# Kernel optimization log

Measured on AMD Instinct MI355X. Metric: run time of the kernel, lower is better.

## Reference

```python
import jax, jax.numpy as jnp
import numpy as np

D_MODEL = 1024
NUM_HEADS = 16
D_K = D_MODEL // NUM_HEADS
THETA = 10000.0
BATCH, SEQ = 2, 2048


def _rope(xh, pos):
    # xh: (..., h, s, d_k), pos: (s,) int
    half = D_K // 2
    inv_freq = THETA ** (-jnp.arange(half, dtype=jnp.float32) * 2.0 / D_K)  # (half,)
    ang = pos.astype(jnp.float32)[:, None] * inv_freq[None, :]              # (s, half)
    cos, sin = jnp.cos(ang), jnp.sin(ang)
    x1 = xh[..., 0::2]  # (..., h, s, half)
    x2 = xh[..., 1::2]
    r1 = x1 * cos - x2 * sin
    r2 = x1 * sin + x2 * cos
    out = jnp.stack([r1, r2], axis=-1)            # (..., h, s, half, 2)
    return out.reshape(xh.shape)


def setup_inputs() -> dict:
    key = jax.random.key(0)
    k1, k2, k3 = jax.random.split(key, 3)
    scale_qkv = (6.0 / (3 * D_MODEL + D_MODEL)) ** 0.5  # xavier uniform bound
    scale_o = (6.0 / (2 * D_MODEL)) ** 0.5
    return {
        "x": jax.random.normal(k1, (BATCH, SEQ, D_MODEL), dtype=jnp.float32),
        "token_positions": jnp.arange(SEQ, dtype=jnp.int64 if jax.config.jax_enable_x64 else jnp.int32),
        "qkv_proj": jax.random.uniform(k2, (3 * D_MODEL, D_MODEL), jnp.float32, -scale_qkv, scale_qkv),
        "o_proj": jax.random.uniform(k3, (D_MODEL, D_MODEL), jnp.float32, -scale_o, scale_o),
    }


def reference(x, token_positions, qkv_proj, o_proj):
    # fused QKV projection: x @ qkv_proj^T
    qkv = jnp.einsum('bsd,ed->bse', x, qkv_proj)          # (b, s, 3*d_model)
    q, k, v = jnp.split(qkv, 3, axis=-1)

    def to_heads(t):
        b, s, _ = t.shape
        return t.reshape(b, s, NUM_HEADS, D_K).transpose(0, 2, 1, 3)  # (b, h, s, d_k)

    qh, kh, vh = to_heads(q), to_heads(k), to_heads(v)
    qh = _rope(qh, token_positions)
    kh = _rope(kh, token_positions)

    scores = jnp.einsum('bhqd,bhkd->bhqk', qh, kh) / (D_K ** 0.5)
    s = x.shape[-2]
    causal = jnp.tril(jnp.ones((s, s), dtype=bool))
    scores = jnp.where(causal, scores, -jnp.inf)
    attn = jax.nn.softmax(scores, axis=-1)
    out = jnp.einsum('bhqk,bhkd->bhqd', attn, vh)          # (b, h, s, d_k)
    out = out.transpose(0, 2, 1, 3).reshape(x.shape[0], s, D_MODEL)
    return jnp.einsum('bsd,od->bso', out, o_proj)
```

## Files before the change

kernel.cpp:

```cpp
#include <hip/hip_runtime.h>
#include <hip/hip_bf16.h>
#include <math.h>

typedef __bf16 bf16_t;
typedef __attribute__((ext_vector_type(2))) __bf16 bf16x2;
typedef __attribute__((ext_vector_type(4))) __bf16 bf16x4;
typedef __attribute__((ext_vector_type(8))) __bf16 bf16x8;
typedef __attribute__((ext_vector_type(4))) float f32x4;

#define BATCH  2
#define SEQ    2048
#define DMODEL 1024
#define NHEADS 16
#define DK     64

typedef const __attribute__((address_space(1))) void* gas_t;
typedef __attribute__((address_space(3))) void* las_t;

#define X_N (BATCH * SEQ * DMODEL)
#define W_N (3 * DMODEL * DMODEL)
#define O_N (DMODEL * DMODEL)

__global__ __launch_bounds__(256) void convert_kernel(
    const float* __restrict__ x, const float* __restrict__ w, const float* __restrict__ o,
    bf16_t* __restrict__ xb, bf16_t* __restrict__ wb, bf16_t* __restrict__ ob)
{
    const int gid = blockIdx.x * 256 + threadIdx.x;
    const float* src; bf16_t* dst; int base = gid * 8;
    if (base < X_N)                { src = x; dst = xb; }
    else if (base < X_N + W_N)     { src = w; dst = wb; base -= X_N; }
    else                           { src = o; dst = ob; base -= X_N + W_N; }
    const f32x4 lo = *(const f32x4*)(src + base);
    const f32x4 hi = *(const f32x4*)(src + base + 4);
    bf16x8 r;
    r[0] = (bf16_t)lo[0]; r[1] = (bf16_t)lo[1]; r[2] = (bf16_t)lo[2]; r[3] = (bf16_t)lo[3];
    r[4] = (bf16_t)hi[0]; r[5] = (bf16_t)hi[1]; r[6] = (bf16_t)hi[2]; r[7] = (bf16_t)hi[3];
    *(bf16x8*)(dst + base) = r;
}

__global__ __launch_bounds__(512) void qkv_gemm_kernel(
    const bf16_t* __restrict__ x, const bf16_t* __restrict__ w,
    const int* __restrict__ pos,
    bf16_t* __restrict__ qo, bf16_t* __restrict__ ko, bf16_t* __restrict__ vt)
{
    __shared__ bf16_t Abuf[2][256 * 64];
    __shared__ bf16_t Bbuf[2][192 * 64];

    const int tid  = threadIdx.x;
    const int lane = tid & 63;
    const int l15  = lane & 15, quad = lane >> 4;
    const int l7   = l15 & 7;
    const int wv   = tid >> 6;
    const int wr   = wv >> 2;
    const int wc   = wv & 3;

    const int bid = blockIdx.x;
    const int xcd = bid & 7, tt = bid >> 3;
    const int yh  = xcd >> 1, ch = xcd & 1;
    const int bx  = ch * 8 + (tt & 7);
    const int by  = yh * 4 + (tt >> 3);
    const int rowBase = by * 256;
    const int colBase = bx * 192;

    const int r0   = tid >> 3;
    const int scol = ((tid & 7) ^ (r0 & 7)) * 8;
    const bf16_t* Ax = x + (size_t)(rowBase + r0) * DMODEL + scol;
    const bf16_t* Bx = w + (size_t)(colBase + r0) * DMODEL + scol;

    f32x4 acc[8][3] = {};

#define STAGE(kt, bufi)                                                          \
    {                                                                            \
        const int k0_ = (kt) * 64;                                               \
        _Pragma("unroll")                                                        \
        for (int l = 0; l < 4; ++l)                                              \
            __builtin_amdgcn_global_load_lds(                                    \
                (gas_t)(Ax + (size_t)(l * 64) * DMODEL + k0_),                   \
                (las_t)(&Abuf[bufi][(l * 512 + tid) * 8]), 16, 0, 0);            \
        _Pragma("unroll")                                                        \
        for (int l = 0; l < 3; ++l)                                              \
            __builtin_amdgcn_global_load_lds(                                    \
                (gas_t)(Bx + (size_t)(l * 64) * DMODEL + k0_),                   \
                (las_t)(&Bbuf[bufi][(l * 512 + tid) * 8]), 16, 0, 0);            \
    }

    STAGE(0, 0)
    STAGE(1, 1)
    asm volatile("s_waitcnt vmcnt(7)" ::: "memory");
    __builtin_amdgcn_s_barrier();
    __builtin_amdgcn_sched_barrier(0);

    for (int t = 0; t < 16; ++t) {
        const int buf = t & 1;
#pragma unroll
        for (int kk = 0; kk < 2; ++kk) {
            const int sw = ((kk * 4 + quad) ^ l7) * 8;
            bf16x8 bfr[3];
#pragma unroll
            for (int j = 0; j < 3; ++j)
                bfr[j] = *(const bf16x8*)&Bbuf[buf][(wc * 48 + j * 16 + l15) * 64 + sw];
            __builtin_amdgcn_s_setprio(1);
#pragma unroll
            for (int i = 0; i < 8; ++i) {
                const bf16x8 af = *(const bf16x8*)&Abuf[buf][(wr * 128 + i * 16 + l15) * 64 + sw];
#pragma unroll
                for (int j = 0; j < 3; ++j)
                    acc[i][j] = __builtin_amdgcn_mfma_f32_16x16x32_bf16(af, bfr[j], acc[i][j], 0, 0, 0);
            }
            __builtin_amdgcn_s_setprio(0);
        }
        __builtin_amdgcn_s_barrier();
        __builtin_amdgcn_sched_barrier(0);
        if (t + 2 < 16) {
            STAGE(t + 2, buf)
            asm volatile("s_waitcnt vmcnt(7)" ::: "memory");
        } else {
            asm volatile("s_waitcnt vmcnt(0)" ::: "memory");
        }
        __builtin_amdgcn_s_barrier();
        __builtin_amdgcn_sched_barrier(0);
    }
#undef STAGE

#pragma unroll
    for (int j = 0; j < 3; ++j) {
        const int colj = colBase + wc * 48 + j * 16;
        const int part = colj >> 10;
        const int h    = (colj & 1023) >> 6;
        const int d    = (colj & 63) + l15;
        bf16_t* op = (part == 0) ? qo : (part == 1) ? ko : vt;
        if (part < 2) {
            const float invf  = exp2f(-(float)(d >> 1) * 0.4152410118609203f);
            const float psign = (d & 1) ? 1.f : -1.f;
#pragma unroll
            for (int i = 0; i < 8; ++i) {
#pragma unroll
                for (int r = 0; r < 4; ++r) {
                    const int m = rowBase + wr * 128 + i * 16 + quad * 4 + r;
                    const int b = m >> 11;
                    const int s = m & (SEQ - 1);
                    const float ang = (float)pos[s] * invf;
                    const float sn_ = __sinf(ang);
                    const float c_  = __cosf(ang);
                    const float v = acc[i][j][r];
                    const float p = __shfl_xor(v, 1);
                    const float res = fmaf(p, psign * sn_, v * c_);
                    op[((size_t)(b * NHEADS + h) * SEQ + s) * DK + d] = (bf16_t)res;
                }
            }
        } else {
#pragma unroll
            for (int i = 0; i < 8; ++i) {
#pragma unroll
                for (int r = 0; r < 4; ++r) {
                    const int m = rowBase + wr * 128 + i * 16 + quad * 4 + r;
                    const int b = m >> 11;
                    const int s = m & (SEQ - 1);
                    const int sp = (s & ~63) | ((s & 15) << 2) | ((s >> 4) & 3);
                    op[(size_t)(b * NHEADS + h) * SEQ * DK + (size_t)d * SEQ + sp]
                        = (bf16_t)acc[i][j][r];
                }
            }
        }
    }
}

__global__ __launch_bounds__(256) void out_gemm_kernel(
    const bf16_t* __restrict__ a, const bf16_t* __restrict__ w, float* __restrict__ out)
{
    __shared__ bf16_t ldsA[2 * 128 * 64];
    __shared__ bf16_t ldsB[2 * 64 * 64];
    const int tid  = threadIdx.x;
    const int lane = tid & 63;
    const int l15  = lane & 15, quad = lane >> 4;
    const int l7   = l15 & 7;
    const int wv   = tid >> 6;
    const int bid = blockIdx.x;
    const int xcd = bid & 7, t = bid >> 3;
    const int xh  = xcd >> 2, yh = xcd & 3;
    const int bx  = xh * 8 + (t & 7);
    const int by  = yh * 8 + (t >> 3);
    const int rowBase = by * 128;
    const int colBase = bx * 64;

    const int sr   = tid >> 3;
    const int scol = ((tid & 7) ^ (sr & 7)) * 8;
    const bf16_t* ga = a + (size_t)(rowBase + sr) * DMODEL + scol;
    const bf16_t* gb = w + (size_t)(colBase + sr) * DMODEL + scol;
    const int dd = tid * 8;

#pragma unroll
    for (int u = 0; u < 4; ++u)
        __builtin_amdgcn_global_load_lds((gas_t)(ga + (size_t)u * 32 * DMODEL),
                                         (las_t)(ldsA + dd + u * 2048), 16, 0, 0);
#pragma unroll
    for (int u = 0; u < 2; ++u)
        __builtin_amdgcn_global_load_lds((gas_t)(gb + (size_t)u * 32 * DMODEL),
                                         (las_t)(ldsB + dd + u * 2048), 16, 0, 0);
    __syncthreads();

    f32x4 acc[2][4] = {};
    int buf = 0;
    for (int k0 = 0; k0 < DMODEL; k0 += 64) {
        if (k0 + 64 < DMODEL) {
            const int offA = (buf ^ 1) * 8192, offB = (buf ^ 1) * 4096;
#pragma unroll
            for (int u = 0; u < 4; ++u)
                __builtin_amdgcn_global_load_lds((gas_t)(ga + k0 + 64 + (size_t)u * 32 * DMODEL),
                                                 (las_t)(ldsA + offA + dd + u * 2048), 16, 0, 0);
#pragma unroll
            for (int u = 0; u < 2; ++u)
                __builtin_amdgcn_global_load_lds((gas_t)(gb + k0 + 64 + (size_t)u * 32 * DMODEL),
                                                 (las_t)(ldsB + offB + dd + u * 2048), 16, 0, 0);
        }
        const bf16_t* La = ldsA + buf * 8192;
        const bf16_t* Lb = ldsB + buf * 4096;
#pragma unroll
        for (int kk = 0; kk < 2; ++kk) {
            const int sw = ((kk * 4 + quad) ^ l7) * 8;
            bf16x8 af[2], bfr[4];
#pragma unroll
            for (int i = 0; i < 2; ++i)
                af[i] = *(const bf16x8*)&La[(wv * 32 + i * 16 + l15) * 64 + sw];
#pragma unroll
            for (int j = 0; j < 4; ++j)
                bfr[j] = *(const bf16x8*)&Lb[(j * 16 + l15) * 64 + sw];
#pragma unroll
            for (int i = 0; i < 2; ++i)
#pragma unroll
                for (int j = 0; j < 4; ++j)
                    acc[i][j] = __builtin_amdgcn_mfma_f32_16x16x32_bf16(af[i], bfr[j], acc[i][j], 0, 0, 0);
        }
        __syncthreads();
        buf ^= 1;
    }
#pragma unroll
    for (int i = 0; i < 2; ++i) {
#pragma unroll
        for (int r = 0; r < 4; ++r) {
            const int m = rowBase + wv * 32 + i * 16 + quad * 4 + r;
#pragma unroll
            for (int j = 0; j < 4; ++j)
                out[(size_t)m * DMODEL + colBase + j * 16 + l15] = acc[i][j][r];
        }
    }
}

__global__ __launch_bounds__(256) void attn_kernel(
    const bf16_t* __restrict__ Q, const bf16_t* __restrict__ K,
    const bf16_t* __restrict__ VT, bf16_t* __restrict__ AO)
{
    __shared__ bf16_t Kb[64 * 64];
    __shared__ bf16_t Vb[64 * 64];
    __shared__ bf16_t Pb[4][16 * 72];

    const int bh = blockIdx.x & 31;
    const int j  = blockIdx.x >> 5;
    const int lo = j & 7, hi = j >> 3;
    const int qb = (hi == 0) ? lo
                 : (hi == 1) ? (31 - lo)
                 : (hi == 2) ? (8 + lo)
                 :             (23 - lo);
    const int nt = qb + 1;

    const int tid  = threadIdx.x;
    const int wave = tid >> 6, lane = tid & 63;
    const int l15  = lane & 15, quad = lane >> 4;
    const int q0   = qb * 64 + wave * 16;
    const size_t hb = (size_t)bh * SEQ * DK;

    const int r0 = tid >> 3;
    const int sc = ((tid & 7) ^ (r0 & 7)) * 8;
    const int dd0 = tid * 8, dd1 = (tid + 256) * 8;

    bf16x8 aq0, aq1;
    {
        const bf16_t* qrow = Q + hb + (size_t)(q0 + l15) * DK + quad * 8;
        aq0 = *(const bf16x8*)qrow;
        aq1 = *(const bf16x8*)(qrow + 32);
#pragma unroll
        for (int i = 0; i < 8; ++i) {
            aq0[i] = (bf16_t)((float)aq0[i] * 0.125f);
            aq1[i] = (bf16_t)((float)aq1[i] * 0.125f);
        }
    }

    f32x4 oacc[4] = {};
    float lsum[4] = {};
    const int swA = (quad ^ (l15 & 7)) * 8;
    const int swB = ((4 + quad) ^ (l15 & 7)) * 8;

    for (int kb = 0; kb < nt; ++kb) {
        __syncthreads();
        {
            const bf16_t* kg = K  + hb + (size_t)kb * 64 * DK + (size_t)r0 * DK  + sc;
            const bf16_t* vg = VT + hb + kb * 64 + (size_t)r0 * SEQ + sc;
            __builtin_amdgcn_global_load_lds((gas_t)kg,              (las_t)(&Kb[dd0]), 16, 0, 0);
            __builtin_amdgcn_global_load_lds((gas_t)(kg + 32 * DK),  (las_t)(&Kb[dd1]), 16, 0, 0);
            __builtin_amdgcn_global_load_lds((gas_t)vg,              (las_t)(&Vb[dd0]), 16, 0, 0);
            __builtin_amdgcn_global_load_lds((gas_t)(vg + 32 * SEQ), (las_t)(&Vb[dd1]), 16, 0, 0);
        }
        __syncthreads();

        const bool nm = (kb == qb);

        bf16x8 kf0[4], kf1[4];
#pragma unroll
        for (int c = 0; c < 4; ++c) {
            kf0[c] = *(const bf16x8*)&Kb[(c * 16 + l15) * 64 + swA];
            kf1[c] = *(const bf16x8*)&Kb[(c * 16 + l15) * 64 + swB];
        }
        f32x4 sc4[4];
#pragma unroll
        for (int c = 0; c < 4; ++c) {
            f32x4 z = {};
            z = __builtin_amdgcn_mfma_f32_16x16x32_bf16(aq0, kf0[c], z, 0, 0, 0);
            z = __builtin_amdgcn_mfma_f32_16x16x32_bf16(aq1, kf1[c], z, 0, 0, 0);
            sc4[c] = z;
        }
#pragma unroll
        for (int r = 0; r < 4; ++r) {
            bf16x4 pr;
#pragma unroll
            for (int c = 0; c < 4; ++c) {
                float s = sc4[c][r];
                if (nm) {
                    const int key = kb * 64 + c * 16 + l15;
                    const int qa  = q0 + quad * 4 + r;
                    s = (key <= qa) ? s : -INFINITY;
                }
                const float p = __expf(s - 8.0f);
                lsum[r] += p;
                pr[c] = (bf16_t)p;
            }
            *(bf16x4*)&Pb[wave][(quad * 4 + r) * 72 + l15 * 4] = pr;
        }
        asm volatile("s_waitcnt lgkmcnt(0)" ::: "memory");

        const bf16x8 ap0 = *(const bf16x8*)&Pb[wave][l15 * 72 + quad * 8];
        const bf16x8 ap1 = *(const bf16x8*)&Pb[wave][l15 * 72 + 32 + quad * 8];
#pragma unroll
        for (int t = 0; t < 4; ++t) {
            const bf16x8 bv0 = *(const bf16x8*)&Vb[(t * 16 + l15) * 64 + swA];
            const bf16x8 bv1 = *(const bf16x8*)&Vb[(t * 16 + l15) * 64 + swB];
            oacc[t] = __builtin_amdgcn_mfma_f32_16x16x32_bf16(ap0, bv0, oacc[t], 0, 0, 0);
            oacc[t] = __builtin_amdgcn_mfma_f32_16x16x32_bf16(ap1, bv1, oacc[t], 0, 0, 0);
        }
    }

    const int b = bh >> 4, h = bh & 15;
    float inv[4];
#pragma unroll
    for (int r = 0; r < 4; ++r) {
        float s = lsum[r];
        s += __shfl_xor(s, 1);
        s += __shfl_xor(s, 2);
        s += __shfl_xor(s, 4);
        s += __shfl_xor(s, 8);
        inv[r] = 1.0f / s;
    }
#pragma unroll
    for (int t = 0; t < 4; ++t)
#pragma unroll
        for (int r = 0; r < 4; ++r) {
            const int qa = q0 + quad * 4 + r;
            AO[(size_t)(b * SEQ + qa) * DMODEL + h * 64 + t * 16 + l15] =
                (bf16_t)(oacc[t][r] * inv[r]);
        }
}

extern "C" void kernel_launch(void* const* d_in, const int* in_sizes, int n_in,
                              void* d_out, int out_size, void* d_ws, size_t ws_size,
                              hipStream_t stream) {
    (void)in_sizes; (void)n_in; (void)out_size; (void)ws_size;
    const float* x    = (const float*)d_in[0];
    const int*   pos  = (const int*)d_in[1];
    const float* qkvw = (const float*)d_in[2];
    const float* ow   = (const float*)d_in[3];
    float* out = (float*)d_out;

    const size_t HEAD_ELEMS = (size_t)BATCH * NHEADS * SEQ * DK;
    bf16_t* Qw  = (bf16_t*)d_ws;
    bf16_t* Kw  = Qw + HEAD_ELEMS;
    bf16_t* Vt  = Kw + HEAD_ELEMS;
    bf16_t* AO  = Vt + HEAD_ELEMS;
    bf16_t* xb  = AO;
    bf16_t* wb  = AO + X_N;
    bf16_t* ob  = wb + W_N;

    convert_kernel<<<dim3(4096), 256, 0, stream>>>(x, qkvw, ow, xb, wb, ob);
    qkv_gemm_kernel<<<dim3(256), 512, 0, stream>>>(xb, wb, pos, Qw, Kw, Vt);
    attn_kernel<<<dim3(1024), 256, 0, stream>>>(Qw, Kw, Vt, AO);
    out_gemm_kernel<<<dim3(512), 256, 0, stream>>>(AO, ob, out);
}
```

Before: 172.2 us.

## Prefetch two stages ahead with vmcnt waits in out-GEMM and attention kernels

The out-projection GEMM now issues loads two K-tiles ahead. It waits on vmcnt counts with raw s_barrier instead of a full __syncthreads drain, and raises wave priority around the MFMA block. The attention kernel gains double-buffered K/V LDS tiles with the same two-ahead prefetch, so global loads overlap with the QK/PV MFMAs instead of stalling each iteration. This adds LDS use and a second barrier per iteration, and relies on vmcnt accounting being correct for the global_load_lds ops.

```diff
diff --git a/kernel.cpp b/kernel.cpp
--- a/kernel.cpp
+++ b/kernel.cpp
@@ -176,10 +176,10 @@
     const int l7   = l15 & 7;
     const int wv   = tid >> 6;
     const int bid = blockIdx.x;
-    const int xcd = bid & 7, t = bid >> 3;
+    const int xcd = bid & 7, t0 = bid >> 3;
     const int xh  = xcd >> 2, yh = xcd & 3;
-    const int bx  = xh * 8 + (t & 7);
-    const int by  = yh * 8 + (t >> 3);
+    const int bx  = xh * 8 + (t0 & 7);
+    const int by  = yh * 8 + (t0 >> 3);
     const int rowBase = by * 128;
     const int colBase = bx * 64;
 
@@ -189,30 +189,30 @@
     const bf16_t* gb = w + (size_t)(colBase + sr) * DMODEL + scol;
     const int dd = tid * 8;
 
-#pragma unroll
-    for (int u = 0; u < 4; ++u)
-        __builtin_amdgcn_global_load_lds((gas_t)(ga + (size_t)u * 32 * DMODEL),
-                                         (las_t)(ldsA + dd + u * 2048), 16, 0, 0);
-#pragma unroll
-    for (int u = 0; u < 2; ++u)
-        __builtin_amdgcn_global_load_lds((gas_t)(gb + (size_t)u * 32 * DMODEL),
-                                         (las_t)(ldsB + dd + u * 2048), 16, 0, 0);
-    __syncthreads();
+#define OSTAGE(kt, bufi)                                                         \
+    {                                                                            \
+        const int k0_ = (kt) * 64;                                               \
+        _Pragma("unroll")                                                        \
+        for (int u = 0; u < 4; ++u)                                              \
+            __builtin_amdgcn_global_load_lds(                                    \
+                (gas_t)(ga + k0_ + (size_t)u * 32 * DMODEL),                     \
+                (las_t)(ldsA + (bufi) * 8192 + dd + u * 2048), 16, 0, 0);        \
+        _Pragma("unroll")                                                        \
+        for (int u = 0; u < 2; ++u)                                              \
+            __builtin_amdgcn_global_load_lds(                                    \
+                (gas_t)(gb + k0_ + (size_t)u * 32 * DMODEL),                     \
+                (las_t)(ldsB + (bufi) * 4096 + dd + u * 2048), 16, 0, 0);        \
+    }
+
+    OSTAGE(0, 0)
+    OSTAGE(1, 1)
+    asm volatile("s_waitcnt vmcnt(6)" ::: "memory");
+    __builtin_amdgcn_s_barrier();
+    __builtin_amdgcn_sched_barrier(0);
 
     f32x4 acc[2][4] = {};
-    int buf = 0;
-    for (int k0 = 0; k0 < DMODEL; k0 += 64) {
-        if (k0 + 64 < DMODEL) {
-            const int offA = (buf ^ 1) * 8192, offB = (buf ^ 1) * 4096;
-#pragma unroll
-            for (int u = 0; u < 4; ++u)
-                __builtin_amdgcn_global_load_lds((gas_t)(ga + k0 + 64 + (size_t)u * 32 * DMODEL),
-                                                 (las_t)(ldsA + offA + dd + u * 2048), 16, 0, 0);
-#pragma unroll
-            for (int u = 0; u < 2; ++u)
-                __builtin_amdgcn_global_load_lds((gas_t)(gb + k0 + 64 + (size_t)u * 32 * DMODEL),
-                                                 (las_t)(ldsB + offB + dd + u * 2048), 16, 0, 0);
-        }
+    for (int t = 0; t < 16; ++t) {
+        const int buf = t & 1;
         const bf16_t* La = ldsA + buf * 8192;
         const bf16_t* Lb = ldsB + buf * 4096;
 #pragma unroll
@@ -225,15 +225,27 @@
 #pragma unroll
             for (int j = 0; j < 4; ++j)
                 bfr[j] = *(const bf16x8*)&Lb[(j * 16 + l15) * 64 + sw];
+            __builtin_amdgcn_s_setprio(1);
 #pragma unroll
             for (int i = 0; i < 2; ++i)
 #pragma unroll
                 for (int j = 0; j < 4; ++j)
                     acc[i][j] = __builtin_amdgcn_mfma_f32_16x16x32_bf16(af[i], bfr[j], acc[i][j], 0, 0, 0);
-        }
-        __syncthreads();
-        buf ^= 1;
-    }
+            __builtin_amdgcn_s_setprio(0);
+        }
+        __builtin_amdgcn_s_barrier();
+        __builtin_amdgcn_sched_barrier(0);
+        if (t + 2 < 16) {
+            OSTAGE(t + 2, buf)
+            asm volatile("s_waitcnt vmcnt(6)" ::: "memory");
+        } else {
+            asm volatile("s_waitcnt vmcnt(0)" ::: "memory");
+        }
+        __builtin_amdgcn_s_barrier();
+        __builtin_amdgcn_sched_barrier(0);
+    }
+#undef OSTAGE
+
 #pragma unroll
     for (int i = 0; i < 2; ++i) {
 #pragma unroll
@@ -250,8 +262,8 @@
     const bf16_t* __restrict__ Q, const bf16_t* __restrict__ K,
     const bf16_t* __restrict__ VT, bf16_t* __restrict__ AO)
 {
-    __shared__ bf16_t Kb[64 * 64];
-    __shared__ bf16_t Vb[64 * 64];
+    __shared__ bf16_t Kb[2][64 * 64];
+    __shared__ bf16_t Vb[2][64 * 64];
     __shared__ bf16_t Pb[4][16 * 72];
 
     const int bh = blockIdx.x & 31;
@@ -290,25 +302,35 @@
     const int swA = (quad ^ (l15 & 7)) * 8;
     const int swB = ((4 + quad) ^ (l15 & 7)) * 8;
 
+#define ASTAGE(kt, bufi)                                                         \
+    {                                                                            \
+        const bf16_t* kg_ = K  + hb + (size_t)(kt) * 64 * DK + (size_t)r0 * DK  + sc; \
+        const bf16_t* vg_ = VT + hb + (kt) * 64 + (size_t)r0 * SEQ + sc;         \
+        __builtin_amdgcn_global_load_lds((gas_t)kg_,              (las_t)(&Kb[bufi][dd0]), 16, 0, 0); \
+        __builtin_amdgcn_global_load_lds((gas_t)(kg_ + 32 * DK),  (las_t)(&Kb[bufi][dd1]), 16, 0, 0); \
+        __builtin_amdgcn_global_load_lds((gas_t)vg_,              (las_t)(&Vb[bufi][dd0]), 16, 0, 0); \
+        __builtin_amdgcn_global_load_lds((gas_t)(vg_ + 32 * SEQ), (las_t)(&Vb[bufi][dd1]), 16, 0, 0); \
+    }
+
+    ASTAGE(0, 0)
+    if (nt > 1) {
+        ASTAGE(1, 1)
+        asm volatile("s_waitcnt vmcnt(4)" ::: "memory");
+    } else {
+        asm volatile("s_waitcnt vmcnt(0)" ::: "memory");
+    }
+    __builtin_amdgcn_s_barrier();
+    __builtin_amdgcn_sched_barrier(0);
+
     for (int kb = 0; kb < nt; ++kb) {
-        __syncthreads();
-        {
-            const bf16_t* kg = K  + hb + (size_t)kb * 64 * DK + (size_t)r0 * DK  + sc;
-            const bf16_t* vg = VT + hb + kb * 64 + (size_t)r0 * SEQ + sc;
-            __builtin_amdgcn_global_load_lds((gas_t)kg,              (las_t)(&Kb[dd0]), 16, 0, 0);
-            __builtin_amdgcn_global_load_lds((gas_t)(kg + 32 * DK),  (las_t)(&Kb[dd1]), 16, 0, 0);
-            __builtin_amdgcn_global_load_lds((gas_t)vg,              (las_t)(&Vb[dd0]), 16, 0, 0);
-            __builtin_amdgcn_global_load_lds((gas_t)(vg + 32 * SEQ), (las_t)(&Vb[dd1]), 16, 0, 0);
-        }
-        __syncthreads();
-
+        const int buf = kb & 1;
         const bool nm = (kb == qb);
 
         bf16x8 kf0[4], kf1[4];
 #pragma unroll
         for (int c = 0; c < 4; ++c) {
-            kf0[c] = *(const bf16x8*)&Kb[(c * 16 + l15) * 64 + swA];
-            kf1[c] = *(const bf16x8*)&Kb[(c * 16 + l15) * 64 + swB];
+            kf0[c] = *(const bf16x8*)&Kb[buf][(c * 16 + l15) * 64 + swA];
+            kf1[c] = *(const bf16x8*)&Kb[buf][(c * 16 + l15) * 64 + swB];
         }
         f32x4 sc4[4];
 #pragma unroll
@@ -341,12 +363,24 @@
         const bf16x8 ap1 = *(const bf16x8*)&Pb[wave][l15 * 72 + 32 + quad * 8];
 #pragma unroll
         for (int t = 0; t < 4; ++t) {
-            const bf16x8 bv0 = *(const bf16x8*)&Vb[(t * 16 + l15) * 64 + swA];
-            const bf16x8 bv1 = *(const bf16x8*)&Vb[(t * 16 + l15) * 64 + swB];
+            const bf16x8 bv0 = *(const bf16x8*)&Vb[buf][(t * 16 + l15) * 64 + swA];
+            const bf16x8 bv1 = *(const bf16x8*)&Vb[buf][(t * 16 + l15) * 64 + swB];
             oacc[t] = __builtin_amdgcn_mfma_f32_16x16x32_bf16(ap0, bv0, oacc[t], 0, 0, 0);
             oacc[t] = __builtin_amdgcn_mfma_f32_16x16x32_bf16(ap1, bv1, oacc[t], 0, 0, 0);
         }
-    }
+
+        __builtin_amdgcn_s_barrier();
+        __builtin_amdgcn_sched_barrier(0);
+        if (kb + 2 < nt) {
+            ASTAGE(kb + 2, buf)
+            asm volatile("s_waitcnt vmcnt(4)" ::: "memory");
+        } else {
+            asm volatile("s_waitcnt vmcnt(0)" ::: "memory");
+        }
+        __builtin_amdgcn_s_barrier();
+        __builtin_amdgcn_sched_barrier(0);
+    }
+#undef ASTAGE
 
     const int b = bh >> 4, h = bh & 15;
     float inv[4];
```

Measured after the change: 169.6 us. Within noise of the previous version (-1.5%).
